# Kernel optimization log

Hardware: AMD Instinct MI355X
Metric: run time of the kernel (lower is better)

The kernel has to match this reference:

```python
import jax, jax.numpy as jnp
import numpy as np

N = 10000   # nodes
E = 160000  # edges (before self-loops)
IN = 77     # input feature dim
H = 4       # heads (layers 1,2)
C = 128     # per-head out channels


def setup_inputs() -> dict:
    key = jax.random.key(0)
    ks = jax.random.split(key, 16)
    p = lambda k, shape: (jax.random.normal(k, shape, jnp.float32) * 0.1)
    z = lambda n: jnp.zeros((n,), jnp.float32)
    return {
        "x": jax.random.normal(ks[0], (N, IN), jnp.float32),
        "edge_index": jax.random.randint(ks[1], (2, E), 0, N),
        # layer 1: 77 -> H*C
        "Wl1": p(ks[2], (H * C, IN)), "bl1": z(H * C),
        "Wr1": p(ks[3], (H * C, IN)), "br1": z(H * C),
        "att1": p(ks[4], (H, C)), "b1": z(H * C),
        # layer 2: H*C -> H*C
        "Wl2": p(ks[5], (H * C, H * C)), "bl2": z(H * C),
        "Wr2": p(ks[6], (H * C, H * C)), "br2": z(H * C),
        "att2": p(ks[7], (H, C)), "b2": z(H * C),
        # layer 3: H*C -> C (1 head)
        "Wl3": p(ks[8], (C, H * C)), "bl3": z(C),
        "Wr3": p(ks[9], (C, H * C)), "br3": z(C),
        "att3": p(ks[10], (1, C)), "b3": z(C),
    }


def _gatv2_layer(x, src, dst, Wl, bl, Wr, br, att, bias, heads, outc):
    """PyG GATv2Conv (eval mode, self-loops already in src/dst, concat=True)."""
    n = x.shape[0]
    xl = (x @ Wl.T + bl).reshape(n, heads, outc)  # source transform
    xr = (x @ Wr.T + br).reshape(n, heads, outc)  # target transform
    # edge-wise score: a^T LeakyReLU(xl[src] + xr[dst])
    e = jax.nn.leaky_relu(xl[src] + xr[dst], negative_slope=0.2)  # [E,H,C]
    logits = jnp.einsum('ehc,hc->eh', e, att)                      # [E,H]
    # segment softmax over edges grouped by destination node
    m = jax.lax.stop_gradient(jax.ops.segment_max(logits, dst, num_segments=n))
    ev = jnp.exp(logits - m[dst])
    denom = jax.ops.segment_sum(ev, dst, num_segments=n)
    alpha = ev / (denom[dst] + 1e-16)                              # [E,H]
    # scatter-add weighted messages
    out = jax.ops.segment_sum(xl[src] * alpha[:, :, None], dst, num_segments=n)
    return out.reshape(n, heads * outc) + bias


def reference(x, edge_index, Wl1, bl1, Wr1, br1, att1, b1,
              Wl2, bl2, Wr2, br2, att2, b2,
              Wl3, bl3, Wr3, br3, att3, b3):
    n = x.shape[0]
    loop = jnp.arange(n)
    src = jnp.concatenate([edge_index[0], loop])  # add self-loops (PyG default)
    dst = jnp.concatenate([edge_index[1], loop])
    h = jax.nn.elu(_gatv2_layer(x, src, dst, Wl1, bl1, Wr1, br1, att1, b1, H, C))
    h = jax.nn.elu(_gatv2_layer(h, src, dst, Wl2, bl2, Wr2, br2, att2, b2, H, C))
    return _gatv2_layer(h, src, dst, Wl3, bl3, Wr3, br3, att3, b3, 1, C)
```

## Files before the change

kernel.cpp:

```cpp
#include <hip/hip_runtime.h>
#include <hip/hip_bf16.h>
#include <math.h>

typedef __attribute__((ext_vector_type(8))) short short8;
typedef __attribute__((ext_vector_type(4))) float f32x4;
typedef __attribute__((ext_vector_type(2))) float f32x2;
typedef __attribute__((ext_vector_type(4))) unsigned int u32x4;

__device__ __forceinline__ float bf2f(unsigned short u) {
  union { unsigned int i; float f; } x; x.i = ((unsigned int)u) << 16; return x.f;
}

__device__ __forceinline__ f32x2 pk_add(f32x2 a, f32x2 b) {
  f32x2 d; asm("v_pk_add_f32 %0, %1, %2" : "=v"(d) : "v"(a), "v"(b)); return d;
}
__device__ __forceinline__ f32x2 pk_mul(f32x2 a, f32x2 b) {
  f32x2 d; asm("v_pk_mul_f32 %0, %1, %2" : "=v"(d) : "v"(a), "v"(b)); return d;
}
__device__ __forceinline__ f32x2 pk_fma(f32x2 a, f32x2 b, f32x2 c) {
  f32x2 d; asm("v_pk_fma_f32 %0, %1, %2, %3" : "=v"(d) : "v"(a), "v"(b), "v"(c)); return d;
}
__device__ __forceinline__ f32x2 pk_abs(f32x2 a) {
  union { f32x2 f; unsigned int u[2]; } x; x.f = a;
  x.u[0] &= 0x7fffffffu; x.u[1] &= 0x7fffffffu;
  return x.f;
}
__device__ __forceinline__ f32x2 unpk(unsigned int w) {
  union { f32x2 f; unsigned int u[2]; } x;
  x.u[0] = w << 16;
  x.u[1] = w & 0xffff0000u;
  return x.f;
}

template <int CTRL>
__device__ __forceinline__ float dpp_add(float x) {
  int y = __builtin_amdgcn_update_dpp(0, __builtin_bit_cast(int, x), CTRL, 0xF, 0xF, true);
  return x + __builtin_bit_cast(float, y);
}
__device__ __forceinline__ float row16_sum(float p) {
  p = dpp_add<0xB1>(p);
  p = dpp_add<0x4E>(p);
  p = dpp_add<0x124>(p);
  p = dpp_add<0x128>(p);
  return p;
}

__device__ __forceinline__ void load_lds16(const void* g, void* l) {
  __builtin_amdgcn_global_load_lds(
      (const __attribute__((address_space(1))) unsigned int*)g,
      (__attribute__((address_space(3))) unsigned int*)l, 16, 0, 0);
}

__global__ __launch_bounds__(256) void gemm_mfma(
    const __hip_bfloat16* __restrict__ A, const __hip_bfloat16* __restrict__ B,
    const float* __restrict__ bl, const float* __restrict__ br, int halfN,
    __hip_bfloat16* __restrict__ out, int M, int K, int Nout) {
  __shared__ __hip_bfloat16 As[128 * 32];
  __shared__ __hip_bfloat16 Bs[128 * 32];
  int t = threadIdx.x;
  int w = t >> 6, l = t & 63;
  int lr = l & 15, lh = l >> 4;
  int wr = w >> 1, wc = w & 1;
  int m0 = blockIdx.y * 128, n0 = blockIdx.x * 128;
  f32x4 acc[4][4] = {};
  int nk = K >> 5;
  for (int ks = 0; ks < nk; ++ks) {
    int k0 = ks << 5;
#pragma unroll
    for (int p = 0; p < 2; ++p) {
      int c = p * 256 + t;
      int row = c >> 2, sub = c & 3;
      int gm = m0 + row; if (gm >= M) gm = M - 1;
      const __hip_bfloat16* gsrc = A + (size_t)gm * K + k0 + sub * 8;
      char* ldst = (char*)As + (size_t)(p * 256 + w * 64) * 16;
      load_lds16(gsrc, ldst);
    }
#pragma unroll
    for (int p = 0; p < 2; ++p) {
      int c = p * 256 + t;
      int row = c >> 2, sub = c & 3;
      const __hip_bfloat16* gsrc = B + (size_t)(n0 + row) * K + k0 + sub * 8;
      char* ldst = (char*)Bs + (size_t)(p * 256 + w * 64) * 16;
      load_lds16(gsrc, ldst);
    }
    __syncthreads();
    short8 af[4], bf[4];
#pragma unroll
    for (int mt = 0; mt < 4; ++mt)
      af[mt] = *(const short8*)(As + (size_t)(wr * 64 + mt * 16 + lr) * 32 + lh * 8);
#pragma unroll
    for (int nt = 0; nt < 4; ++nt)
      bf[nt] = *(const short8*)(Bs + (size_t)(wc * 64 + nt * 16 + lr) * 32 + lh * 8);
#pragma unroll
    for (int mt = 0; mt < 4; ++mt)
#pragma unroll
      for (int nt = 0; nt < 4; ++nt)
        acc[mt][nt] = __builtin_amdgcn_mfma_f32_16x16x32_bf16(af[mt], bf[nt], acc[mt][nt], 0, 0, 0);
    __syncthreads();
  }
#pragma unroll
  for (int mt = 0; mt < 4; ++mt) {
#pragma unroll
    for (int r = 0; r < 4; ++r) {
      int gm = m0 + wr * 64 + mt * 16 + lh * 4 + r;
      if (gm >= M) continue;
#pragma unroll
      for (int nt = 0; nt < 4; ++nt) {
        int gn = n0 + wc * 64 + nt * 16 + lr;
        float bv = (gn < halfN) ? bl[gn] : br[gn - halfN];
        out[(size_t)gm * Nout + gn] = __float2bfloat16(acc[mt][nt][r] + bv);
      }
    }
  }
}

struct CastSeg { const float* src; __hip_bfloat16* dst; int rows, K, Kp, row0, start; };
struct CastArgs { CastSeg s[7]; int total; };

__global__ __launch_bounds__(256) void k_prep(CastArgs A, const int* __restrict__ ei,
                                              int E, int N, int* __restrict__ deg) {
  int stride = gridDim.x * blockDim.x;
  int tid0 = blockIdx.x * blockDim.x + threadIdx.x;
  for (int i = tid0; i < A.total; i += stride) {
    int si = 0;
#pragma unroll
    for (int j = 1; j < 7; j++) if (i >= A.s[j].start) si = j;
    CastSeg sg = A.s[si];
    int li = i - sg.start;
    int r = li / sg.Kp, k = li - r * sg.Kp;
    float v = (k < sg.K) ? sg.src[(size_t)r * sg.K + k] : 0.f;
    sg.dst[(size_t)(sg.row0 + r) * sg.Kp + k] = __float2bfloat16(v);
  }
  int ET = E + N;
  for (int e = tid0; e < ET; e += stride) {
    int d = (e < E) ? ei[E + e] : (e - E);
    atomicAdd(&deg[d], 1);
  }
}

__global__ __launch_bounds__(256) void k_scan_perm(const int* __restrict__ deg, int N,
                                                   int* __restrict__ rp, int* __restrict__ cursor,
                                                   int* __restrict__ perm) {
  __shared__ int part[256];
  __shared__ int bcnt[64];
  __shared__ int boff[64];
  int t = threadIdx.x;
  int chunk = (N + 255) / 256;
  int lo = t * chunk;
  int hi = lo + chunk; if (hi > N) hi = N;
  int s = 0;
  for (int i = lo; i < hi; ++i) s += deg[i];
  part[t] = s;
  if (t < 64) bcnt[t] = 0;
  __syncthreads();
  for (int off = 1; off < 256; off <<= 1) {
    int x = (t >= off) ? part[t - off] : 0;
    __syncthreads();
    part[t] += x;
    __syncthreads();
  }
  int run = (t == 0) ? 0 : part[t - 1];
  for (int i = lo; i < hi; ++i) {
    rp[i] = run;
    cursor[i] = run;
    run += deg[i];
    int b = deg[i] < 63 ? deg[i] : 63;
    atomicAdd(&bcnt[b], 1);
  }
  if (t == 255) rp[N] = run;
  __syncthreads();
  if (t == 0) {
    int acc = 0;
    for (int b = 63; b >= 0; --b) { boff[b] = acc; acc += bcnt[b]; }
  }
  __syncthreads();
  for (int i = lo; i < hi; ++i) {
    int b = deg[i] < 63 ? deg[i] : 63;
    int pos = atomicAdd(&boff[b], 1);
    perm[pos] = i;
  }
}

__global__ void k_scatter(const int* __restrict__ ei, int E, int N,
                          int* __restrict__ cursor, int* __restrict__ srcs) {
  int e = blockIdx.x * blockDim.x + threadIdx.x;
  int ET = E + N;
  if (e >= ET) return;
  int s = (e < E) ? ei[e] : (e - E);
  int d = (e < E) ? ei[E + e] : (e - E);
  int pos = atomicAdd(&cursor[d], 1);
  srcs[pos] = s;
}

template <int CPL> struct VecSel;
template <> struct VecSel<8> { using T = short8; };
template <> struct VecSel<2> { using T = unsigned int; };

template <int HC, int Hn, int LDc, bool ELU, typename OutT>
__global__ __launch_bounds__(256) void k_edge_fused(
    const __hip_bfloat16* __restrict__ xl, const __hip_bfloat16* __restrict__ xr,
    const int* __restrict__ rp, const int* __restrict__ srcs,
    const int* __restrict__ perm,
    const float* __restrict__ att, const float* __restrict__ bias,
    int N, OutT* __restrict__ out) {
  const int CPL = HC / 64;
  const int NP = CPL / 2;
  using VecT = typename VecSel<CPL>::T;
  int lane = threadIdx.x & 63;
  int nw = (blockIdx.x * blockDim.x + threadIdx.x) >> 6;
  if (nw >= N) return;
  int n = perm[nw];

  f32x2 a06[NP], a04[NP], xrv2[NP];
#pragma unroll
  for (int p = 0; p < NP; ++p) {
    float alo = att[lane * CPL + 2 * p], ahi = att[lane * CPL + 2 * p + 1];
    a06[p].x = 0.6f * alo; a06[p].y = 0.6f * ahi;
    a04[p].x = 0.4f * alo; a04[p].y = 0.4f * ahi;
  }
  {
    const unsigned int* xw = (const unsigned int*)(xr + (size_t)n * LDc + lane * CPL);
#pragma unroll
    for (int p = 0; p < NP; ++p) xrv2[p] = unpk(xw[p]);
  }

  int s0 = rp[n], s1 = rp[n + 1];
  int len = s1 - s0;
  float m = -INFINITY, sum = 0.f;
  f32x2 acc2[NP];
#pragma unroll
  for (int p = 0; p < NP; ++p) { acc2[p].x = 0.f; acc2[p].y = 0.f; }

  auto loadrow = [&](int idx) -> VecT {
    return *(const VecT*)(xl + (size_t)srcs[s0 + idx] * LDc + lane * CPL);
  };
  auto proc = [&](VecT v) {
    unsigned int wv[NP];
    if constexpr (CPL == 8) {
      union { VecT s; u32x4 w; } u; u.s = v;
#pragma unroll
      for (int p = 0; p < NP; ++p) wv[p] = u.w[p];
    } else {
      wv[0] = (unsigned int)v;
    }
    f32x2 xv2[NP];
    f32x2 p2; p2.x = 0.f; p2.y = 0.f;
#pragma unroll
    for (int p = 0; p < NP; ++p) {
      xv2[p] = unpk(wv[p]);
      f32x2 s = pk_add(xv2[p], xrv2[p]);
      f32x2 sa = pk_abs(s);
      p2 = pk_fma(a06[p], s, p2);
      p2 = pk_fma(a04[p], sa, p2);
    }
    float pp = p2.x + p2.y;
    pp = row16_sum(pp);
    if constexpr (Hn == 1) {
      pp += __shfl_xor(pp, 16, 64);
      pp += __shfl_xor(pp, 32, 64);
    }
    if (__any(pp > m + 8.f)) {
      float mn = fmaxf(m, pp);
      float corr = __expf(m - mn);
      float wgt = __expf(pp - mn);
      sum = sum * corr + wgt;
      f32x2 corr2; corr2.x = corr; corr2.y = corr;
      f32x2 wgt2; wgt2.x = wgt; wgt2.y = wgt;
#pragma unroll
      for (int p = 0; p < NP; ++p)
        acc2[p] = pk_fma(acc2[p], corr2, pk_mul(wgt2, xv2[p]));
      m = mn;
    } else {
      float wgt = __expf(pp - m);
      sum += wgt;
      f32x2 wgt2; wgt2.x = wgt; wgt2.y = wgt;
#pragma unroll
      for (int p = 0; p < NP; ++p) acc2[p] = pk_fma(wgt2, xv2[p], acc2[p]);
    }
  };

  if (len > 0) {
    VecT b0, b1;
    b0 = loadrow(0);
    if (len > 1) b1 = loadrow(1);
    int i = 0;
    for (; i + 1 < len; i += 2) {
      VecT n0v, n1v;
      bool pf = (i + 2 < len);
      if (pf) {
        n0v = loadrow(i + 2);
        n1v = (i + 3 < len) ? loadrow(i + 3) : n0v;
      }
      proc(b0);
      proc(b1);
      if (pf) { b0 = n0v; b1 = n1v; }
    }
    if (i < len) proc(b0);
  }

  float inv = 1.f / (sum + 1e-16f);
#pragma unroll
  for (int p = 0; p < NP; ++p) {
    float r0 = acc2[p].x * inv + bias[lane * CPL + 2 * p];
    float r1 = acc2[p].y * inv + bias[lane * CPL + 2 * p + 1];
    if (ELU) {
      r0 = r0 > 0.f ? r0 : expm1f(r0);
      r1 = r1 > 0.f ? r1 : expm1f(r1);
    }
    acc2[p].x = r0; acc2[p].y = r1;
  }
  if constexpr (sizeof(OutT) == 2) {
    short8 o;
#pragma unroll
    for (int p = 0; p < NP; ++p) {
      __hip_bfloat16 b0 = __float2bfloat16(acc2[p].x);
      __hip_bfloat16 b1 = __float2bfloat16(acc2[p].y);
      o[2 * p] = __builtin_bit_cast(short, b0);
      o[2 * p + 1] = __builtin_bit_cast(short, b1);
    }
    *(short8*)((__hip_bfloat16*)out + (size_t)n * HC + lane * CPL) = o;
  } else {
    f32x2 o; o.x = acc2[0].x; o.y = acc2[0].y;
    *(f32x2*)((float*)out + (size_t)n * HC + lane * 2) = o;
  }
}

extern "C" void kernel_launch(void* const* d_in, const int* in_sizes, int n_in,
                              void* d_out, int out_size, void* d_ws, size_t ws_size,
                              hipStream_t stream) {
  const int IN = 77, Kp1 = 96, Hh = 4, Cc = 128, HC = Hh * Cc;
  const int N = in_sizes[0] / IN;
  const int E = in_sizes[1] / 2;
  const int ET = E + N;

  const float* x   = (const float*)d_in[0];
  const int*   ei  = (const int*)d_in[1];
  const float* Wl1 = (const float*)d_in[2];  const float* bl1 = (const float*)d_in[3];
  const float* Wr1 = (const float*)d_in[4];  const float* br1 = (const float*)d_in[5];
  const float* att1= (const float*)d_in[6];  const float* b1  = (const float*)d_in[7];
  const float* Wl2 = (const float*)d_in[8];  const float* bl2 = (const float*)d_in[9];
  const float* Wr2 = (const float*)d_in[10]; const float* br2 = (const float*)d_in[11];
  const float* att2= (const float*)d_in[12]; const float* b2  = (const float*)d_in[13];
  const float* Wl3 = (const float*)d_in[14]; const float* bl3 = (const float*)d_in[15];
  const float* Wr3 = (const float*)d_in[16]; const float* br3 = (const float*)d_in[17];
  const float* att3= (const float*)d_in[18]; const float* b3  = (const float*)d_in[19];
  float* out = (float*)d_out;

  char* w = (char*)d_ws;
  size_t off = 0;
  auto alloc = [&](size_t bytes) -> void* {
    void* p = w + off;
    off += (bytes + 255) & ~(size_t)255;
    return p;
  };
  __hip_bfloat16* xlr = (__hip_bfloat16*)alloc((size_t)N * 2 * HC * 2);
  __hip_bfloat16* hb  = (__hip_bfloat16*)alloc((size_t)N * HC * 2);
  __hip_bfloat16* Wc1 = (__hip_bfloat16*)alloc((size_t)2 * HC * Kp1 * 2);
  __hip_bfloat16* Wc2 = (__hip_bfloat16*)alloc((size_t)2 * HC * HC * 2);
  __hip_bfloat16* Wc3 = (__hip_bfloat16*)alloc((size_t)2 * Cc * HC * 2);
  int*   deg    = (int*)alloc((size_t)N * 4);
  int*   rp     = (int*)alloc((size_t)(N + 1) * 4);
  int*   cursor = (int*)alloc((size_t)N * 4);
  int*   srcs   = (int*)alloc((size_t)ET * 4);
  int*   perm   = (int*)alloc((size_t)N * 4);

  CastArgs CA;
  int cum = 0;
  auto seg = [&](int idx, const float* src, __hip_bfloat16* dst, int rows, int K, int Kp, int row0) {
    CA.s[idx] = {src, dst, rows, K, Kp, row0, cum};
    cum += rows * Kp;
  };
  seg(0, Wl1, Wc1, HC, IN, Kp1, 0);
  seg(1, Wr1, Wc1, HC, IN, Kp1, HC);
  seg(2, Wl2, Wc2, HC, HC, HC, 0);
  seg(3, Wr2, Wc2, HC, HC, HC, HC);
  seg(4, Wl3, Wc3, Cc, HC, HC, 0);
  seg(5, Wr3, Wc3, Cc, HC, HC, Cc);
  seg(6, x,   hb,  N,  IN, Kp1, 0);
  CA.total = cum;

  hipMemsetAsync(deg, 0, (size_t)N * 4, stream);
  k_prep<<<1024, 256, 0, stream>>>(CA, ei, E, N, deg);
  k_scan_perm<<<1, 256, 0, stream>>>(deg, N, rp, cursor, perm);
  k_scatter<<<(ET + 255) / 256, 256, 0, stream>>>(ei, E, N, cursor, srcs);

  int nodeBlocks = (N + 3) / 4;
  int mb = (N + 127) / 128;

  {
    dim3 g(2 * HC / 128, mb);
    gemm_mfma<<<g, 256, 0, stream>>>(hb, Wc1, bl1, br1, HC, xlr, N, Kp1, 2 * HC);
    k_edge_fused<512, 4, 1024, true, __hip_bfloat16><<<nodeBlocks, 256, 0, stream>>>(
        xlr, xlr + HC, rp, srcs, perm, att1, b1, N, hb);
  }
  {
    dim3 g(2 * HC / 128, mb);
    gemm_mfma<<<g, 256, 0, stream>>>(hb, Wc2, bl2, br2, HC, xlr, N, HC, 2 * HC);
    k_edge_fused<512, 4, 1024, true, __hip_bfloat16><<<nodeBlocks, 256, 0, stream>>>(
        xlr, xlr + HC, rp, srcs, perm, att2, b2, N, hb);
  }
  {
    dim3 g(2 * Cc / 128, mb);
    gemm_mfma<<<g, 256, 0, stream>>>(hb, Wc3, bl3, br3, Cc, xlr, N, HC, 2 * Cc);
    k_edge_fused<128, 1, 256, false, float><<<nodeBlocks, 256, 0, stream>>>(
        xlr, xlr + Cc, rp, srcs, perm, att3, b3, N, out);
  }
}
```

Measured before the change: 214.0 us.

## Deepen edge gather pipeline to groups of four with prefetched indices

```diff
diff --git a/kernel.cpp b/kernel.cpp
--- a/kernel.cpp
+++ b/kernel.cpp
@@ -205,6 +205,7 @@
     int N, OutT* __restrict__ out) {
   const int CPL = HC / 64;
   const int NP = CPL / 2;
+  const int G = 4;
   using VecT = typename VecSel<CPL>::T;
   int lane = threadIdx.x & 63;
   int nw = (blockIdx.x * blockDim.x + threadIdx.x) >> 6;
@@ -231,8 +232,8 @@
 #pragma unroll
   for (int p = 0; p < NP; ++p) { acc2[p].x = 0.f; acc2[p].y = 0.f; }
 
-  auto loadrow = [&](int idx) -> VecT {
-    return *(const VecT*)(xl + (size_t)srcs[s0 + idx] * LDc + lane * CPL);
+  auto rowAt = [&](int s) -> VecT {
+    return *(const VecT*)(xl + (size_t)s * LDc + lane * CPL);
   };
   auto proc = [&](VecT v) {
     unsigned int wv[NP];
@@ -279,23 +280,30 @@
     }
   };
 
-  if (len > 0) {
-    VecT b0, b1;
-    b0 = loadrow(0);
-    if (len > 1) b1 = loadrow(1);
-    int i = 0;
-    for (; i + 1 < len; i += 2) {
-      VecT n0v, n1v;
-      bool pf = (i + 2 < len);
-      if (pf) {
-        n0v = loadrow(i + 2);
-        n1v = (i + 3 < len) ? loadrow(i + 3) : n0v;
-      }
-      proc(b0);
-      proc(b1);
-      if (pf) { b0 = n0v; b1 = n1v; }
-    }
-    if (i < len) proc(b0);
+  int ibA[G], ibB[G];
+  VecT rb[G];
+#pragma unroll
+  for (int j = 0; j < G; ++j) ibA[j] = (j < len) ? srcs[s0 + j] : 0;
+#pragma unroll
+  for (int j = 0; j < G; ++j) ibB[j] = (G + j < len) ? srcs[s0 + G + j] : 0;
+#pragma unroll
+  for (int j = 0; j < G; ++j) if (j < len) rb[j] = rowAt(ibA[j]);
+
+  int ngroups = (len + G - 1) / G;
+  for (int g = 0; g < ngroups; ++g) {
+    int gbase = g * G;
+    int nb[G];
+    int base2 = gbase + 2 * G;
+#pragma unroll
+    for (int j = 0; j < G; ++j) nb[j] = (base2 + j < len) ? srcs[s0 + base2 + j] : 0;
+    VecT rn[G];
+    int base1 = gbase + G;
+#pragma unroll
+    for (int j = 0; j < G; ++j) if (base1 + j < len) rn[j] = rowAt(ibB[j]);
+#pragma unroll
+    for (int j = 0; j < G; ++j) if (gbase + j < len) proc(rb[j]);
+#pragma unroll
+    for (int j = 0; j < G; ++j) { ibA[j] = ibB[j]; ibB[j] = nb[j]; rb[j] = rn[j]; }
   }
 
   float inv = 1.f / (sum + 1e-16f);
@@ -361,7 +369,7 @@
   int*   deg    = (int*)alloc((size_t)N * 4);
   int*   rp     = (int*)alloc((size_t)(N + 1) * 4);
   int*   cursor = (int*)alloc((size_t)N * 4);
-  int*   srcs   = (int*)alloc((size_t)ET * 4);
+  int*   srcs   = (int*)alloc((size_t)(ET + 64) * 4);
   int*   perm   = (int*)alloc((size_t)N * 4);
 
   CastArgs CA;
```

New measurement: 210.5 us. About the same (-1.6%).
